# Kernel tuning notes

Measured on AMD Instinct MI355X. Metric: run time of the kernel, lower is better.

The kernel has to match this reference:

```python
import jax, jax.numpy as jnp
import numpy as np

N = 200000   # nodes
E = 6400000  # edges (avg degree 32)
T = 6        # member feature dim
M = 10       # fingerprint dim
L = 4        # R + 1 layers
GIN = 14     # group_level_input
GLO = 10     # group_level_output


def setup_inputs() -> dict:
    key = jax.random.key(0)
    ks = jax.random.split(key, 10)
    return {
        "x_member": jax.random.normal(ks[0], (N, T), dtype=jnp.float32),
        "x_group": jax.random.normal(ks[1], (1, GIN), dtype=jnp.float32),
        "src": jax.random.randint(ks[2], (E,), 0, N, dtype=jnp.int32),
        "dst": jax.random.randint(ks[3], (E,), 0, N, dtype=jnp.int32),
        "H": jax.random.normal(ks[4], (L, T, M), dtype=jnp.float32),
        "W": jax.random.normal(ks[5], (L,), dtype=jnp.float32),
        "gW": jax.random.normal(ks[6], (GLO, GIN), dtype=jnp.float32) * 0.1,
        "gb": jax.random.normal(ks[7], (GLO,), dtype=jnp.float32),
        "mW": jax.random.normal(ks[8], (3, M + GLO), dtype=jnp.float32) * 0.1,
        "mb": jax.random.normal(ks[9], (3,), dtype=jnp.float32),
    }


def reference(x_member, x_group, src, dst, H, W, gW, gb, mW, mb):
    n = x_member.shape[0]
    # message passing: neighbor feature sum per destination node  [N, T]
    neigh = jax.ops.segment_sum(x_member[src], dst, num_segments=n)
    v1 = x_member + neigh  # r[a] + sum of neighbor r's; r is layer-invariant
    # all R+1 layers at once: [L, N, M]
    v2 = jax.nn.sigmoid(jnp.einsum("nt,ltm->lnm", v1, H))
    fl = jax.nn.softmax(v2 * W[:, None, None], axis=-1)
    # f starts at zeros and accumulates softmax over every node and layer -> [1, M]
    f = jnp.sum(fl, axis=(0, 1))[None, :]
    # group-level perceptron
    g = jax.nn.sigmoid(x_group @ gW.T + gb)  # [1, GLO]
    merged = jnp.concatenate([f, g], axis=1)  # [1, M+GLO]
    return jax.nn.softmax(merged @ mW.T + mb, axis=-1)  # [1, 3]
```

## Files before the change

### kernel.cpp

```cpp
#include <hip/hip_runtime.h>
#include <hip/hip_fp16.h>
#include <math.h>

#define TDIM 6
#define MDIM 10
#define LDIM 4
#define GIND 14
#define GLOD 10

#define BINSHIFT 8
#define BINSZ 256
#define MAXBINS 1024

#define SC2_BLOCKS 512
#define SC2_THREADS 512
#define SC2_KQ 7
#define OVF_ENT 16384
#define META2 2048

#define SC_BLOCK 512
#define SC_EPT 32
#define SC_EPB (SC_BLOCK * SC_EPT)
#define AC_BLOCK 512
#define AC_CAP 8704
#define AC_EPT 17

__global__ void zero32_k(unsigned* __restrict__ p, int n) {
    int i = blockIdx.x * blockDim.x + threadIdx.x;
    if (i < n) p[i] = 0u;
}

__device__ __forceinline__ void add_row4(uint4 r, float& s0, float& s1, float& s2,
                                         float& s3, float& s4, float& s5) {
    float2 a0 = __half22float2(*(__half2*)&r.x);
    float2 a1 = __half22float2(*(__half2*)&r.y);
    float2 a2 = __half22float2(*(__half2*)&r.z);
    s0 += a0.x; s1 += a0.y; s2 += a1.x; s3 += a1.y; s4 += a2.x; s5 += a2.y;
}


__global__ __launch_bounds__(SC2_THREADS) void scat2_k(
        const float* __restrict__ xm, int N, uint4* __restrict__ xh,
        const int* __restrict__ src, const int* __restrict__ dst, int E, int NQ, int QPB,
        unsigned* __restrict__ gcount, unsigned* __restrict__ ebuf, int C, int nbins,
        uint2* __restrict__ ovf, unsigned* __restrict__ ocur) {
    __shared__ unsigned lcount[MAXBINS];
    __shared__ unsigned lbase[MAXBINS];
    int tid = threadIdx.x;
    for (int i = tid; i < MAXBINS; i += SC2_THREADS) lcount[i] = 0u;

    int gid = blockIdx.x * SC2_THREADS + tid;
    int gstride = gridDim.x * SC2_THREADS;
    for (int n = gid; n < N; n += gstride) {
        const float2* r = (const float2*)(xm + (size_t)n * TDIM);
        float2 a = r[0], b = r[1], c = r[2];
        __half2 h0 = __floats2half2_rn(a.x, a.y);
        __half2 h1 = __floats2half2_rn(b.x, b.y);
        __half2 h2 = __floats2half2_rn(c.x, c.y);
        uint4 o;
        o.x = *(unsigned*)&h0; o.y = *(unsigned*)&h1; o.z = *(unsigned*)&h2; o.w = 0u;
        xh[n] = o;
    }
    if (blockIdx.x == 0) {
        for (int e = NQ * 4 + tid; e < E; e += SC2_THREADS) {
            unsigned oc = atomicAdd(ocur, 1u);
            if (oc < OVF_ENT) ovf[oc] = make_uint2((unsigned)src[e], (unsigned)dst[e]);
        }
    }
    __syncthreads();

    int qb = blockIdx.x * QPB;
    int qend = qb + QPB; if (qend > NQ) qend = NQ;
    const int4* s4p = (const int4*)src;
    const int4* d4p = (const int4*)dst;

    unsigned pk[SC2_KQ * 4];
    unsigned wr[SC2_KQ * 4];

#pragma unroll
    for (int i = 0; i < SC2_KQ; i++) {
        int q = qb + tid + i * SC2_THREADS;
        if (q < qend) {
            int4 sv = s4p[q];
            int4 dv = d4p[q];
            {
                unsigned du = (unsigned)dv.x, b = du >> BINSHIFT;
                pk[i*4+0] = ((du & (BINSZ-1)) << 18) | (unsigned)sv.x;
                wr[i*4+0] = (b << 18) | atomicAdd(&lcount[b], 1u);
            }
            {
                unsigned du = (unsigned)dv.y, b = du >> BINSHIFT;
                pk[i*4+1] = ((du & (BINSZ-1)) << 18) | (unsigned)sv.y;
                wr[i*4+1] = (b << 18) | atomicAdd(&lcount[b], 1u);
            }
            {
                unsigned du = (unsigned)dv.z, b = du >> BINSHIFT;
                pk[i*4+2] = ((du & (BINSZ-1)) << 18) | (unsigned)sv.z;
                wr[i*4+2] = (b << 18) | atomicAdd(&lcount[b], 1u);
            }
            {
                unsigned du = (unsigned)dv.w, b = du >> BINSHIFT;
                pk[i*4+3] = ((du & (BINSZ-1)) << 18) | (unsigned)sv.w;
                wr[i*4+3] = (b << 18) | atomicAdd(&lcount[b], 1u);
            }
        } else {
            pk[i*4+0] = 0xFFFFFFFFu; pk[i*4+1] = 0xFFFFFFFFu;
            pk[i*4+2] = 0xFFFFFFFFu; pk[i*4+3] = 0xFFFFFFFFu;
        }
    }
    __syncthreads();

    for (int i = tid; i < nbins; i += SC2_THREADS) {
        unsigned c = lcount[i];
        if (c) lbase[i] = atomicAdd(&gcount[i], c);
    }
    __syncthreads();

#pragma unroll
    for (int k = 0; k < SC2_KQ * 4; k++) {
        unsigned p = pk[k];
        if (p != 0xFFFFFFFFu) {
            unsigned b = wr[k] >> 18;
            unsigned pos = lbase[b] + (wr[k] & 0x3FFFFu);
            if (pos < (unsigned)C) {
                ebuf[b * (unsigned)C + pos] = p;
            } else {
                unsigned oc = atomicAdd(ocur, 1u);
                if (oc < OVF_ENT) {
                    unsigned s = p & 0x3FFFFu;
                    unsigned d = (b << BINSHIFT) | (p >> 18);
                    ovf[oc] = make_uint2(s, d);
                }
            }
        }
    }
}

__global__ __launch_bounds__(AC_BLOCK) void accum2_k(
        const float* __restrict__ xm, const uint4* __restrict__ xh,
        const unsigned* __restrict__ ebuf, const unsigned* __restrict__ gcount, int C,
        const unsigned* __restrict__ ocur, const uint2* __restrict__ ovf,
        const float* __restrict__ H, const float* __restrict__ W,
        float* __restrict__ facc, int N) {
    __shared__ unsigned srt[AC_CAP];
    __shared__ unsigned cnt[BINSZ];
    __shared__ unsigned cstart[BINSZ];
    __shared__ unsigned wsum[8];
    __shared__ unsigned ovl[256];
    __shared__ unsigned ovn;
    __shared__ float sH[LDIM * TDIM * MDIM];
    __shared__ float sW[LDIM];
    __shared__ float sred[AC_BLOCK / 64][MDIM];
    __shared__ float part[2][BINSZ][TDIM];
    int tid = threadIdx.x;
    int bin = blockIdx.x;
    for (int i = tid; i < LDIM * TDIM * MDIM; i += AC_BLOCK) sH[i] = H[i];
    if (tid < LDIM) sW[tid] = W[tid];
    if (tid < BINSZ) cnt[tid] = 0u;
    if (tid == 0) ovn = 0u;
    __syncthreads();

    unsigned gc = gcount[bin];
    unsigned m = gc < (unsigned)C ? gc : (unsigned)C;
    unsigned e0 = (unsigned)bin * (unsigned)C;
    int nbase = bin << BINSHIFT;

    unsigned ed_[AC_EPT];
    unsigned rk_[AC_EPT];
#pragma unroll
    for (int k = 0; k < AC_EPT; k++) {
        unsigned i = (unsigned)tid + (unsigned)k * AC_BLOCK;
        if (i < m) {
            unsigned v = __builtin_nontemporal_load(ebuf + e0 + i);
            ed_[k] = v;
            rk_[k] = atomicAdd(&cnt[v >> 18], 1u);
        }
    }
    {
        unsigned novf = *ocur;
        if (novf > OVF_ENT) novf = OVF_ENT;
        for (unsigned i = tid; i < novf; i += AC_BLOCK) {
            uint2 e = ovf[i];
            if ((e.y >> BINSHIFT) == (unsigned)bin) {
                unsigned u = atomicAdd(&ovn, 1u);
                if (u < 256u) ovl[u] = ((e.y & (BINSZ-1)) << 18) | e.x;
            }
        }
    }
    __syncthreads();

    {
        unsigned v = (tid < BINSZ) ? cnt[tid] : 0u;
        int lane = tid & 63;
#pragma unroll
        for (int off = 1; off < 64; off <<= 1) {
            unsigned t = (unsigned)__shfl_up((int)v, off, 64);
            if (lane >= off) v += t;
        }
        if (tid < BINSZ && lane == 63) wsum[tid >> 6] = v;
        __syncthreads();
        if (tid < BINSZ) {
            unsigned add = 0;
            int w = tid >> 6;
#pragma unroll
            for (int ww = 0; ww < 3; ww++) if (ww < w) add += wsum[ww];
            cstart[tid] = v + add - cnt[tid];
        }
        __syncthreads();
    }

#pragma unroll
    for (int k = 0; k < AC_EPT; k++) {
        unsigned i = (unsigned)tid + (unsigned)k * AC_BLOCK;
        if (i < m) {
            unsigned v = ed_[k];
            srt[cstart[v >> 18] + rk_[k]] = v & 0x3FFFFu;
        }
    }
    __syncthreads();

    int node = tid & (BINSZ - 1);
    int role = tid >> 8;
    int n = nbase + node;
    float s0 = 0.f, s1 = 0.f, s2 = 0.f, s3 = 0.f, s4 = 0.f, s5 = 0.f;
    if (n < N) {
        unsigned c = cnt[node];
        unsigned b0 = cstart[node];
        unsigned h = c >> 1;
        unsigned j  = role ? h : 0u;
        unsigned je = role ? c : h;
        for (; j + 8 <= je; j += 8) {
            unsigned i0 = srt[b0 + j],     i1 = srt[b0 + j + 1];
            unsigned i2 = srt[b0 + j + 2], i3 = srt[b0 + j + 3];
            unsigned i4 = srt[b0 + j + 4], i5 = srt[b0 + j + 5];
            unsigned i6 = srt[b0 + j + 6], i7 = srt[b0 + j + 7];
            uint4 r0 = xh[i0], r1 = xh[i1], r2 = xh[i2], r3 = xh[i3];
            uint4 r4 = xh[i4], r5 = xh[i5], r6 = xh[i6], r7 = xh[i7];
            add_row4(r0, s0, s1, s2, s3, s4, s5);
            add_row4(r1, s0, s1, s2, s3, s4, s5);
            add_row4(r2, s0, s1, s2, s3, s4, s5);
            add_row4(r3, s0, s1, s2, s3, s4, s5);
            add_row4(r4, s0, s1, s2, s3, s4, s5);
            add_row4(r5, s0, s1, s2, s3, s4, s5);
            add_row4(r6, s0, s1, s2, s3, s4, s5);
            add_row4(r7, s0, s1, s2, s3, s4, s5);
        }
        for (; j + 2 <= je; j += 2) {
            unsigned ia = srt[b0 + j], ib = srt[b0 + j + 1];
            uint4 ra = xh[ia], rb = xh[ib];
            add_row4(ra, s0, s1, s2, s3, s4, s5);
            add_row4(rb, s0, s1, s2, s3, s4, s5);
        }
        if (j < je) {
            uint4 ra = xh[srt[b0 + j]];
            add_row4(ra, s0, s1, s2, s3, s4, s5);
        }
        if (role == 0) {
            unsigned no = ovn < 256u ? ovn : 256u;
            for (unsigned q = 0; q < no; q++) {
                unsigned o = ovl[q];
                if ((int)(o >> 18) == node) {
                    uint4 rr = xh[o & 0x3FFFFu];
                    add_row4(rr, s0, s1, s2, s3, s4, s5);
                }
            }
        }
    }
    part[role][node][0] = s0; part[role][node][1] = s1; part[role][node][2] = s2;
    part[role][node][3] = s3; part[role][node][4] = s4; part[role][node][5] = s5;
    __syncthreads();

    float fs[MDIM];
#pragma unroll
    for (int mm = 0; mm < MDIM; mm++) fs[mm] = 0.f;

    if (n < N) {
        float v[TDIM];
        const float2* xr = (const float2*)(xm + (size_t)n * TDIM);
        float2 x0 = xr[0], x1 = xr[1], x2 = xr[2];
        v[0] = x0.x + part[0][node][0] + part[1][node][0];
        v[1] = x0.y + part[0][node][1] + part[1][node][1];
        v[2] = x1.x + part[0][node][2] + part[1][node][2];
        v[3] = x1.y + part[0][node][3] + part[1][node][3];
        v[4] = x2.x + part[0][node][4] + part[1][node][4];
        v[5] = x2.y + part[0][node][5] + part[1][node][5];

        int lb = role << 1;
#pragma unroll
        for (int li = 0; li < 2; li++) {
            int l = lb + li;
            float z[MDIM];
#pragma unroll
            for (int mm = 0; mm < MDIM; mm++) {
                float a2 = 0.f;
#pragma unroll
                for (int t = 0; t < TDIM; t++) a2 += v[t] * sH[(l * TDIM + t) * MDIM + mm];
                z[mm] = a2;
            }
            float wl = sW[l];
            float mx = -1e30f;
#pragma unroll
            for (int mm = 0; mm < MDIM; mm++) {
                float sg = wl / (1.f + __expf(-z[mm]));
                z[mm] = sg;
                mx = fmaxf(mx, sg);
            }
            float se = 0.f;
#pragma unroll
            for (int mm = 0; mm < MDIM; mm++) {
                float e = __expf(z[mm] - mx);
                z[mm] = e;
                se += e;
            }
            float inv = 1.f / se;
#pragma unroll
            for (int mm = 0; mm < MDIM; mm++) fs[mm] += z[mm] * inv;
        }
    }

#pragma unroll
    for (int mm = 0; mm < MDIM; mm++) {
        float v = fs[mm];
#pragma unroll
        for (int off = 32; off > 0; off >>= 1) v += __shfl_down(v, off, 64);
        fs[mm] = v;
    }
    int wave = tid >> 6, lane = tid & 63;
    if (lane == 0) {
#pragma unroll
        for (int mm = 0; mm < MDIM; mm++) sred[wave][mm] = fs[mm];
    }
    __syncthreads();
    if (tid < MDIM) {
        float s = 0.f;
#pragma unroll
        for (int w = 0; w < AC_BLOCK / 64; w++) s += sred[w][tid];
        atomicAdd(facc + tid, s);
    }
}


__global__ __launch_bounds__(256) void prep_k(const float* __restrict__ xm, int N,
                                              uint4* __restrict__ xh,
                                              const int* __restrict__ dst, int E,
                                              unsigned* __restrict__ hist, int nbins) {
    __shared__ unsigned lh[MAXBINS];
    for (int i = threadIdx.x; i < MAXBINS; i += blockDim.x) lh[i] = 0u;
    __syncthreads();
    int gid = blockIdx.x * blockDim.x + threadIdx.x;
    int gstride = gridDim.x * blockDim.x;
    for (int n = gid; n < N; n += gstride) {
        const float2* r = (const float2*)(xm + (size_t)n * TDIM);
        float2 a = r[0], b = r[1], c = r[2];
        __half2 h0 = __floats2half2_rn(a.x, a.y);
        __half2 h1 = __floats2half2_rn(b.x, b.y);
        __half2 h2 = __floats2half2_rn(c.x, c.y);
        uint4 o;
        o.x = *(unsigned*)&h0; o.y = *(unsigned*)&h1; o.z = *(unsigned*)&h2; o.w = 0u;
        xh[n] = o;
    }
    int e4 = E >> 2;
    const int4* d4p = (const int4*)dst;
    for (int i = gid; i < e4; i += gstride) {
        int4 d = d4p[i];
        atomicAdd(&lh[((unsigned)d.x) >> BINSHIFT], 1u);
        atomicAdd(&lh[((unsigned)d.y) >> BINSHIFT], 1u);
        atomicAdd(&lh[((unsigned)d.z) >> BINSHIFT], 1u);
        atomicAdd(&lh[((unsigned)d.w) >> BINSHIFT], 1u);
    }
    for (int e = (e4 << 2) + gid; e < E; e += gstride)
        atomicAdd(&lh[((unsigned)dst[e]) >> BINSHIFT], 1u);
    __syncthreads();
    for (int i = threadIdx.x; i < nbins; i += blockDim.x)
        if (lh[i]) atomicAdd(&hist[i], lh[i]);
}

__global__ __launch_bounds__(MAXBINS) void scan_k(const unsigned* __restrict__ hist,
                                                  unsigned* __restrict__ offsets,
                                                  unsigned* __restrict__ gfill, int nbins) {
    __shared__ unsigned buf[2][MAXBINS];
    int t = threadIdx.x;
    buf[0][t] = (t < nbins) ? hist[t] : 0u;
    __syncthreads();
    int cur = 0;
    for (int off = 1; off < MAXBINS; off <<= 1) {
        unsigned v = buf[cur][t];
        if (t >= off) v += buf[cur][t - off];
        buf[cur ^ 1][t] = v;
        __syncthreads();
        cur ^= 1;
    }
    if (t < nbins) {
        unsigned ex = t ? buf[cur][t - 1] : 0u;
        offsets[t] = ex;
        gfill[t] = ex;
    }
    if (t == 0) offsets[nbins] = buf[cur][nbins - 1];
}

__global__ __launch_bounds__(SC_BLOCK) void scatter_k(const int* __restrict__ src,
                                                      const int* __restrict__ dst, int E,
                                                      unsigned* __restrict__ gfill,
                                                      unsigned* __restrict__ ebuf, int nbins) {
    __shared__ unsigned lcount[MAXBINS];
    __shared__ unsigned lbase[MAXBINS];
    for (int i = threadIdx.x; i < MAXBINS; i += SC_BLOCK) lcount[i] = 0u;
    __syncthreads();
    int base = blockIdx.x * SC_EPB + threadIdx.x * SC_EPT;
    int s[SC_EPT], d[SC_EPT];
    unsigned rk[SC_EPT];
#pragma unroll
    for (int q = 0; q < SC_EPT / 4; q++) {
        int e = base + q * 4;
        if (e + 3 < E) {
            int4 s4 = *(const int4*)(src + e);
            int4 d4 = *(const int4*)(dst + e);
            s[q*4+0] = s4.x; s[q*4+1] = s4.y; s[q*4+2] = s4.z; s[q*4+3] = s4.w;
            d[q*4+0] = d4.x; d[q*4+1] = d4.y; d[q*4+2] = d4.z; d[q*4+3] = d4.w;
        } else {
#pragma unroll
            for (int k = 0; k < 4; k++) {
                int ee = e + k;
                s[q*4+k] = (ee < E) ? src[ee] : -1;
                d[q*4+k] = (ee < E) ? dst[ee] : 0;
            }
        }
    }
#pragma unroll
    for (int k = 0; k < SC_EPT; k++)
        if (s[k] >= 0) rk[k] = atomicAdd(&lcount[((unsigned)d[k]) >> BINSHIFT], 1u);
    __syncthreads();
    for (int i = threadIdx.x; i < nbins; i += SC_BLOCK) {
        unsigned c = lcount[i];
        if (c) lbase[i] = atomicAdd(&gfill[i], c);
    }
    __syncthreads();
#pragma unroll
    for (int k = 0; k < SC_EPT; k++) {
        if (s[k] >= 0) {
            unsigned du = (unsigned)d[k];
            unsigned b = du >> BINSHIFT;
            unsigned pack = ((du & (BINSZ - 1)) << 18) | (unsigned)s[k];
            ebuf[lbase[b] + rk[k]] = pack;
        }
    }
}

__global__ __launch_bounds__(AC_BLOCK) void accum_node_k(
        const float* __restrict__ xm, const uint4* __restrict__ xh,
        const unsigned* __restrict__ ebuf, const unsigned* __restrict__ offsets,
        const float* __restrict__ H, const float* __restrict__ W,
        float* __restrict__ facc, int N) {
    __shared__ unsigned srt[AC_CAP];
    __shared__ unsigned cnt[BINSZ];
    __shared__ unsigned tmp[BINSZ];
    __shared__ unsigned cstart[BINSZ];
    __shared__ float sH[LDIM * TDIM * MDIM];
    __shared__ float sW[LDIM];
    __shared__ float sred[AC_BLOCK / 64][MDIM];
    int tid = threadIdx.x;
    int bin = blockIdx.x;
    for (int i = tid; i < LDIM * TDIM * MDIM; i += AC_BLOCK) sH[i] = H[i];
    if (tid < LDIM) sW[tid] = W[tid];
    if (tid < BINSZ) cnt[tid] = 0u;
    __syncthreads();

    unsigned e0 = offsets[bin], e1 = offsets[bin + 1];
    unsigned total = e1 - e0;
    unsigned m = total < AC_CAP ? total : AC_CAP;
    int nbase = bin << BINSHIFT;

    unsigned ed_[AC_EPT];
    unsigned rk_[AC_EPT];
#pragma unroll
    for (int k = 0; k < AC_EPT; k++) {
        unsigned idx = e0 + (unsigned)tid + (unsigned)k * AC_BLOCK;
        if (idx < e0 + m) {
            unsigned v = ebuf[idx];
            ed_[k] = v;
            rk_[k] = atomicAdd(&cnt[v >> 18], 1u);
        }
    }
    __syncthreads();

    if (tid < BINSZ) tmp[tid] = cnt[tid];
    __syncthreads();
    for (int off = 1; off < BINSZ; off <<= 1) {
        unsigned v = 0;
        if (tid < BINSZ) { v = tmp[tid]; if (tid >= off) v += tmp[tid - off]; }
        __syncthreads();
        if (tid < BINSZ) tmp[tid] = v;
        __syncthreads();
    }
    if (tid < BINSZ) cstart[tid] = tmp[tid] - cnt[tid];
    __syncthreads();

#pragma unroll
    for (int k = 0; k < AC_EPT; k++) {
        unsigned idx = e0 + (unsigned)tid + (unsigned)k * AC_BLOCK;
        if (idx < e0 + m) {
            unsigned v = ed_[k];
            srt[cstart[v >> 18] + rk_[k]] = v & 0x3FFFFu;
        }
    }
    __syncthreads();

    float fs[MDIM];
#pragma unroll
    for (int mm = 0; mm < MDIM; mm++) fs[mm] = 0.f;

    int n = nbase + tid;
    if (tid < BINSZ && n < N) {
        float s0 = 0.f, s1 = 0.f, s2 = 0.f, s3 = 0.f, s4 = 0.f, s5 = 0.f;
        unsigned c = cnt[tid];
        unsigned b0 = cstart[tid];
        unsigned j = 0;
        for (; j + 2 <= c; j += 2) {
            unsigned sa = srt[b0 + j], sb = srt[b0 + j + 1];
            uint4 ra = xh[sa];
            uint4 rb = xh[sb];
            add_row4(ra, s0, s1, s2, s3, s4, s5);
            add_row4(rb, s0, s1, s2, s3, s4, s5);
        }
        if (j < c) {
            uint4 ra = xh[srt[b0 + j]];
            add_row4(ra, s0, s1, s2, s3, s4, s5);
        }
        for (unsigned idx = e0 + m; idx < e1; idx++) {
            unsigned v = ebuf[idx];
            if ((int)(v >> 18) == tid) {
                uint4 ra = xh[v & 0x3FFFFu];
                add_row4(ra, s0, s1, s2, s3, s4, s5);
            }
        }

        float v[TDIM];
        const float2* xr = (const float2*)(xm + (size_t)n * TDIM);
        float2 x0 = xr[0], x1 = xr[1], x2 = xr[2];
        v[0] = x0.x + s0; v[1] = x0.y + s1;
        v[2] = x1.x + s2; v[3] = x1.y + s3;
        v[4] = x2.x + s4; v[5] = x2.y + s5;

#pragma unroll
        for (int l = 0; l < LDIM; l++) {
            float z[MDIM];
#pragma unroll
            for (int mm = 0; mm < MDIM; mm++) {
                float a2 = 0.f;
#pragma unroll
                for (int t = 0; t < TDIM; t++) a2 += v[t] * sH[(l * TDIM + t) * MDIM + mm];
                z[mm] = a2;
            }
            float wl = sW[l];
            float mx = -1e30f;
#pragma unroll
            for (int mm = 0; mm < MDIM; mm++) {
                float sg = wl / (1.f + __expf(-z[mm]));
                z[mm] = sg;
                mx = fmaxf(mx, sg);
            }
            float se = 0.f;
#pragma unroll
            for (int mm = 0; mm < MDIM; mm++) {
                float e = __expf(z[mm] - mx);
                z[mm] = e;
                se += e;
            }
            float inv = 1.f / se;
#pragma unroll
            for (int mm = 0; mm < MDIM; mm++) fs[mm] += z[mm] * inv;
        }
    }

#pragma unroll
    for (int mm = 0; mm < MDIM; mm++) {
        float v = fs[mm];
#pragma unroll
        for (int off = 32; off > 0; off >>= 1) v += __shfl_down(v, off, 64);
        fs[mm] = v;
    }
    int wave = tid >> 6, lane = tid & 63;
    if (lane == 0) {
#pragma unroll
        for (int mm = 0; mm < MDIM; mm++) sred[wave][mm] = fs[mm];
    }
    __syncthreads();
    if (tid < MDIM) {
        float s = 0.f;
#pragma unroll
        for (int w = 0; w < AC_BLOCK / 64; w++) s += sred[w][tid];
        atomicAdd(facc + tid, s);
    }
}

__global__ void finalize_k(const float* __restrict__ facc,
                           const float* __restrict__ xg,
                           const float* __restrict__ gW,
                           const float* __restrict__ gb,
                           const float* __restrict__ mW,
                           const float* __restrict__ mb,
                           float* __restrict__ out) {
    if (threadIdx.x == 0 && blockIdx.x == 0) {
        float merged[MDIM + GLOD];
#pragma unroll
        for (int m = 0; m < MDIM; m++) merged[m] = facc[m];
        for (int j = 0; j < GLOD; j++) {
            float a = gb[j];
            for (int i = 0; i < GIND; i++) a += xg[i] * gW[j * GIND + i];
            merged[MDIM + j] = 1.f / (1.f + __expf(-a));
        }
        float lg[3];
        float mx = -1e30f;
        for (int k = 0; k < 3; k++) {
            float a = mb[k];
            for (int j = 0; j < MDIM + GLOD; j++) a += merged[j] * mW[k * (MDIM + GLOD) + j];
            lg[k] = a;
            mx = fmaxf(mx, a);
        }
        float se = 0.f;
        for (int k = 0; k < 3; k++) { lg[k] = __expf(lg[k] - mx); se += lg[k]; }
        float inv = 1.f / se;
        for (int k = 0; k < 3; k++) out[k] = lg[k] * inv;
    }
}

__global__ void fb_zero_k(float* __restrict__ ws, int n) {
    int i = blockIdx.x * blockDim.x + threadIdx.x;
    if (i < n) ws[i] = 0.f;
}

__global__ void fb_edge_scatter_k(const float* __restrict__ xm,
                                  const int* __restrict__ src,
                                  const int* __restrict__ dst,
                                  float* __restrict__ neigh, int E) {
    int e = blockIdx.x * blockDim.x + threadIdx.x;
    if (e >= E) return;
    int s = src[e], d = dst[e];
    const float2* r = (const float2*)(xm + (size_t)s * TDIM);
    float2 a = r[0], b = r[1], c = r[2];
    float* o = neigh + (size_t)d * TDIM;
    atomicAdd(o + 0, a.x); atomicAdd(o + 1, a.y);
    atomicAdd(o + 2, b.x); atomicAdd(o + 3, b.y);
    atomicAdd(o + 4, c.x); atomicAdd(o + 5, c.y);
}

__global__ __launch_bounds__(256) void fb_node_k(
        const float* __restrict__ xm, const float* __restrict__ neigh,
        const float* __restrict__ H, const float* __restrict__ W,
        float* __restrict__ facc, int N) {
    __shared__ float sH[LDIM * TDIM * MDIM];
    __shared__ float sW[LDIM];
    __shared__ float sred[4][MDIM];
    int tid = threadIdx.x;
    for (int i = tid; i < LDIM * TDIM * MDIM; i += blockDim.x) sH[i] = H[i];
    if (tid < LDIM) sW[tid] = W[tid];
    __syncthreads();
    float fs[MDIM];
#pragma unroll
    for (int m = 0; m < MDIM; m++) fs[m] = 0.f;
    for (int n = blockIdx.x * blockDim.x + tid; n < N; n += gridDim.x * blockDim.x) {
        float v[TDIM];
        const float2* xr = (const float2*)(xm + (size_t)n * TDIM);
        const float2* nr = (const float2*)(neigh + (size_t)n * TDIM);
#pragma unroll
        for (int t2 = 0; t2 < 3; t2++) {
            float2 a = xr[t2], b = nr[t2];
            v[2 * t2 + 0] = a.x + b.x;
            v[2 * t2 + 1] = a.y + b.y;
        }
#pragma unroll
        for (int l = 0; l < LDIM; l++) {
            float z[MDIM];
#pragma unroll
            for (int m = 0; m < MDIM; m++) {
                float a2 = 0.f;
#pragma unroll
                for (int t = 0; t < TDIM; t++) a2 += v[t] * sH[(l * TDIM + t) * MDIM + m];
                z[m] = a2;
            }
            float wl = sW[l], mx = -1e30f;
#pragma unroll
            for (int m = 0; m < MDIM; m++) { float sg = wl / (1.f + __expf(-z[m])); z[m] = sg; mx = fmaxf(mx, sg); }
            float se = 0.f;
#pragma unroll
            for (int m = 0; m < MDIM; m++) { float e = __expf(z[m] - mx); z[m] = e; se += e; }
            float inv = 1.f / se;
#pragma unroll
            for (int m = 0; m < MDIM; m++) fs[m] += z[m] * inv;
        }
    }
#pragma unroll
    for (int m = 0; m < MDIM; m++) {
        float v = fs[m];
#pragma unroll
        for (int off = 32; off > 0; off >>= 1) v += __shfl_down(v, off, 64);
        fs[m] = v;
    }
    int wave = tid >> 6, lane = tid & 63;
    if (lane == 0) {
#pragma unroll
        for (int m = 0; m < MDIM; m++) sred[wave][m] = fs[m];
    }
    __syncthreads();
    if (tid < MDIM) {
        float s = sred[0][tid] + sred[1][tid] + sred[2][tid] + sred[3][tid];
        atomicAdd(facc + tid, s);
    }
}

extern "C" void kernel_launch(void* const* d_in, const int* in_sizes, int n_in,
                              void* d_out, int out_size, void* d_ws, size_t ws_size,
                              hipStream_t stream) {
    const float* xm  = (const float*)d_in[0];
    const float* xg  = (const float*)d_in[1];
    const int*   src = (const int*)d_in[2];
    const int*   dst = (const int*)d_in[3];
    const float* H   = (const float*)d_in[4];
    const float* W   = (const float*)d_in[5];
    const float* gW  = (const float*)d_in[6];
    const float* gb  = (const float*)d_in[7];
    const float* mW  = (const float*)d_in[8];
    const float* mb  = (const float*)d_in[9];
    float* out = (float*)d_out;

    int N = in_sizes[0] / TDIM;
    int E = in_sizes[2];
    int nbins = (N + BINSZ - 1) >> BINSHIFT;
    size_t ws_words = ws_size / 4;
    size_t xh_words = (size_t)N * 4;

    long fixed = (long)(xh_words + META2 + (size_t)OVF_ENT * 2);
    long avail = (long)ws_words - fixed;
    long C = avail > 0 ? (avail / nbins) & ~3L : 0;
    if (C > AC_CAP) C = AC_CAP;
    double mu = (double)E / nbins;
    long Cmin = (long)(mu + 4.0 * sqrt(mu) + 32.0);
    int NQ = E >> 2;
    int QPB = (NQ + SC2_BLOCKS - 1) / SC2_BLOCKS;
    bool ok1 = (C >= Cmin) && nbins <= MAXBINS && N <= (1 << 18) &&
               QPB <= SC2_KQ * SC2_THREADS;

    size_t meta_words2 = MAXBINS + (MAXBINS + 1) + MAXBINS + 16;
    size_t need2 = (xh_words + (size_t)E + meta_words2) * 4;
    bool ok2 = ws_size >= need2 && nbins <= MAXBINS && N <= (1 << 18);

    if (ok1) {
        uint4*    xh     = (uint4*)d_ws;
        unsigned* ebuf   = (unsigned*)d_ws + xh_words;
        unsigned* gcount = ebuf + (size_t)nbins * C;
        unsigned* ocur   = gcount + MAXBINS;
        float*    facc   = (float*)(ocur + 16);
        uint2*    ovf    = (uint2*)(gcount + META2);

        zero32_k<<<(META2 + 255) / 256, 256, 0, stream>>>(gcount, META2);
        scat2_k<<<SC2_BLOCKS, SC2_THREADS, 0, stream>>>(xm, N, xh, src, dst, E, NQ, QPB,
                                                        gcount, ebuf, (int)C, nbins, ovf, ocur);
        accum2_k<<<nbins, AC_BLOCK, 0, stream>>>(xm, xh, ebuf, gcount, (int)C, ocur, ovf,
                                                 H, W, facc, N);
        finalize_k<<<1, 64, 0, stream>>>(facc, xg, gW, gb, mW, mb, out);
    } else if (ok2) {
        uint4*    xh      = (uint4*)d_ws;
        unsigned* ebuf    = (unsigned*)d_ws + xh_words;
        unsigned* hist    = ebuf + (size_t)E;
        unsigned* offsets = hist + MAXBINS;
        unsigned* gfill   = offsets + MAXBINS + 1;
        float*    facc    = (float*)(gfill + MAXBINS);

        zero32_k<<<(int)((meta_words2 + 255) / 256), 256, 0, stream>>>(hist, (int)meta_words2);
        prep_k<<<1024, 256, 0, stream>>>(xm, N, xh, dst, E, hist, nbins);
        scan_k<<<1, MAXBINS, 0, stream>>>(hist, offsets, gfill, nbins);
        scatter_k<<<(E + SC_EPB - 1) / SC_EPB, SC_BLOCK, 0, stream>>>(src, dst, E, gfill, ebuf, nbins);
        accum_node_k<<<nbins, AC_BLOCK, 0, stream>>>(xm, xh, ebuf, offsets, H, W, facc, N);
        finalize_k<<<1, 64, 0, stream>>>(facc, xg, gW, gb, mW, mb, out);
    } else {
        float* neigh = (float*)d_ws;
        float* facc  = neigh + (size_t)N * TDIM;
        int zn = N * TDIM + 16;
        fb_zero_k<<<(zn + 255) / 256, 256, 0, stream>>>(neigh, zn);
        fb_edge_scatter_k<<<(E + 255) / 256, 256, 0, stream>>>(xm, src, dst, neigh, E);
        fb_node_k<<<256, 256, 0, stream>>>(xm, neigh, H, W, facc, N);
        finalize_k<<<1, 64, 0, stream>>>(facc, xg, gW, gb, mW, mb, out);
    }
}
```

Measured before the change: 135.2 us.

## Halve bin size and split each node's edges across four threads

Bins shrink from 256 to 128 nodes, doubling the number of bins and accum blocks, with shared sort capacity and per-thread edge slots scaled down to match. Each node is now handled by four threads: each gathers a quarter of the node's neighbor list and then computes one of the four layers. This is meant to raise parallelism and cut the per-thread gather latency chain and shared memory per block. The scan kernel is rewritten to handle two bins per thread so it can cover 2048 bins. It risks a higher overflow rate because per-bin capacity headroom changes, plus more blocks and more scatter-stage metadata.

Result: slower. 148.7 us (+9.9%).

```diff
diff --git a/kernel.cpp b/kernel.cpp
--- a/kernel.cpp
+++ b/kernel.cpp
@@ -8,22 +8,22 @@
 #define GIND 14
 #define GLOD 10
 
-#define BINSHIFT 8
-#define BINSZ 256
-#define MAXBINS 1024
+#define BINSHIFT 7
+#define BINSZ 128
+#define MAXBINS 2048
 
 #define SC2_BLOCKS 512
 #define SC2_THREADS 512
 #define SC2_KQ 7
 #define OVF_ENT 16384
-#define META2 2048
+#define META2 4096
 
 #define SC_BLOCK 512
 #define SC_EPT 32
 #define SC_EPB (SC_BLOCK * SC_EPT)
 #define AC_BLOCK 512
-#define AC_CAP 8704
-#define AC_EPT 17
+#define AC_CAP 4480
+#define AC_EPT 9
 
 __global__ void zero32_k(unsigned* __restrict__ p, int n) {
     int i = blockIdx.x * blockDim.x + threadIdx.x;
@@ -145,13 +145,13 @@
     __shared__ unsigned srt[AC_CAP];
     __shared__ unsigned cnt[BINSZ];
     __shared__ unsigned cstart[BINSZ];
-    __shared__ unsigned wsum[8];
+    __shared__ unsigned wsum[BINSZ / 64];
     __shared__ unsigned ovl[256];
     __shared__ unsigned ovn;
     __shared__ float sH[LDIM * TDIM * MDIM];
     __shared__ float sW[LDIM];
     __shared__ float sred[AC_BLOCK / 64][MDIM];
-    __shared__ float part[2][BINSZ][TDIM];
+    __shared__ float part[4][BINSZ][TDIM];
     int tid = threadIdx.x;
     int bin = blockIdx.x;
     for (int i = tid; i < LDIM * TDIM * MDIM; i += AC_BLOCK) sH[i] = H[i];
@@ -203,7 +203,7 @@
             unsigned add = 0;
             int w = tid >> 6;
 #pragma unroll
-            for (int ww = 0; ww < 3; ww++) if (ww < w) add += wsum[ww];
+            for (int ww = 0; ww < BINSZ / 64 - 1; ww++) if (ww < w) add += wsum[ww];
             cstart[tid] = v + add - cnt[tid];
         }
         __syncthreads();
@@ -220,38 +220,24 @@
     __syncthreads();
 
     int node = tid & (BINSZ - 1);
-    int role = tid >> 8;
+    int role = tid >> 7;
     int n = nbase + node;
     float s0 = 0.f, s1 = 0.f, s2 = 0.f, s3 = 0.f, s4 = 0.f, s5 = 0.f;
     if (n < N) {
         unsigned c = cnt[node];
         unsigned b0 = cstart[node];
-        unsigned h = c >> 1;
-        unsigned j  = role ? h : 0u;
-        unsigned je = role ? c : h;
-        for (; j + 8 <= je; j += 8) {
+        unsigned j  = (c * (unsigned)role) >> 2;
+        unsigned je = (c * (unsigned)(role + 1)) >> 2;
+        for (; j + 4 <= je; j += 4) {
             unsigned i0 = srt[b0 + j],     i1 = srt[b0 + j + 1];
             unsigned i2 = srt[b0 + j + 2], i3 = srt[b0 + j + 3];
-            unsigned i4 = srt[b0 + j + 4], i5 = srt[b0 + j + 5];
-            unsigned i6 = srt[b0 + j + 6], i7 = srt[b0 + j + 7];
             uint4 r0 = xh[i0], r1 = xh[i1], r2 = xh[i2], r3 = xh[i3];
-            uint4 r4 = xh[i4], r5 = xh[i5], r6 = xh[i6], r7 = xh[i7];
             add_row4(r0, s0, s1, s2, s3, s4, s5);
             add_row4(r1, s0, s1, s2, s3, s4, s5);
             add_row4(r2, s0, s1, s2, s3, s4, s5);
             add_row4(r3, s0, s1, s2, s3, s4, s5);
-            add_row4(r4, s0, s1, s2, s3, s4, s5);
-            add_row4(r5, s0, s1, s2, s3, s4, s5);
-            add_row4(r6, s0, s1, s2, s3, s4, s5);
-            add_row4(r7, s0, s1, s2, s3, s4, s5);
-        }
-        for (; j + 2 <= je; j += 2) {
-            unsigned ia = srt[b0 + j], ib = srt[b0 + j + 1];
-            uint4 ra = xh[ia], rb = xh[ib];
-            add_row4(ra, s0, s1, s2, s3, s4, s5);
-            add_row4(rb, s0, s1, s2, s3, s4, s5);
-        }
-        if (j < je) {
+        }
+        for (; j < je; ++j) {
             uint4 ra = xh[srt[b0 + j]];
             add_row4(ra, s0, s1, s2, s3, s4, s5);
         }
@@ -278,44 +264,40 @@
         float v[TDIM];
         const float2* xr = (const float2*)(xm + (size_t)n * TDIM);
         float2 x0 = xr[0], x1 = xr[1], x2 = xr[2];
-        v[0] = x0.x + part[0][node][0] + part[1][node][0];
-        v[1] = x0.y + part[0][node][1] + part[1][node][1];
-        v[2] = x1.x + part[0][node][2] + part[1][node][2];
-        v[3] = x1.y + part[0][node][3] + part[1][node][3];
-        v[4] = x2.x + part[0][node][4] + part[1][node][4];
-        v[5] = x2.y + part[0][node][5] + part[1][node][5];
-
-        int lb = role << 1;
-#pragma unroll
-        for (int li = 0; li < 2; li++) {
-            int l = lb + li;
-            float z[MDIM];
-#pragma unroll
-            for (int mm = 0; mm < MDIM; mm++) {
-                float a2 = 0.f;
-#pragma unroll
-                for (int t = 0; t < TDIM; t++) a2 += v[t] * sH[(l * TDIM + t) * MDIM + mm];
-                z[mm] = a2;
-            }
-            float wl = sW[l];
-            float mx = -1e30f;
-#pragma unroll
-            for (int mm = 0; mm < MDIM; mm++) {
-                float sg = wl / (1.f + __expf(-z[mm]));
-                z[mm] = sg;
-                mx = fmaxf(mx, sg);
-            }
-            float se = 0.f;
-#pragma unroll
-            for (int mm = 0; mm < MDIM; mm++) {
-                float e = __expf(z[mm] - mx);
-                z[mm] = e;
-                se += e;
-            }
-            float inv = 1.f / se;
-#pragma unroll
-            for (int mm = 0; mm < MDIM; mm++) fs[mm] += z[mm] * inv;
-        }
+        v[0] = x0.x + part[0][node][0] + part[1][node][0] + part[2][node][0] + part[3][node][0];
+        v[1] = x0.y + part[0][node][1] + part[1][node][1] + part[2][node][1] + part[3][node][1];
+        v[2] = x1.x + part[0][node][2] + part[1][node][2] + part[2][node][2] + part[3][node][2];
+        v[3] = x1.y + part[0][node][3] + part[1][node][3] + part[2][node][3] + part[3][node][3];
+        v[4] = x2.x + part[0][node][4] + part[1][node][4] + part[2][node][4] + part[3][node][4];
+        v[5] = x2.y + part[0][node][5] + part[1][node][5] + part[2][node][5] + part[3][node][5];
+
+        int l = role;
+        float z[MDIM];
+#pragma unroll
+        for (int mm = 0; mm < MDIM; mm++) {
+            float a2 = 0.f;
+#pragma unroll
+            for (int t = 0; t < TDIM; t++) a2 += v[t] * sH[(l * TDIM + t) * MDIM + mm];
+            z[mm] = a2;
+        }
+        float wl = sW[l];
+        float mx = -1e30f;
+#pragma unroll
+        for (int mm = 0; mm < MDIM; mm++) {
+            float sg = wl / (1.f + __expf(-z[mm]));
+            z[mm] = sg;
+            mx = fmaxf(mx, sg);
+        }
+        float se = 0.f;
+#pragma unroll
+        for (int mm = 0; mm < MDIM; mm++) {
+            float e = __expf(z[mm] - mx);
+            z[mm] = e;
+            se += e;
+        }
+        float inv = 1.f / se;
+#pragma unroll
+        for (int mm = 0; mm < MDIM; mm++) fs[mm] += z[mm] * inv;
     }
 
 #pragma unroll
@@ -375,27 +357,28 @@
         if (lh[i]) atomicAdd(&hist[i], lh[i]);
 }
 
-__global__ __launch_bounds__(MAXBINS) void scan_k(const unsigned* __restrict__ hist,
-                                                  unsigned* __restrict__ offsets,
-                                                  unsigned* __restrict__ gfill, int nbins) {
-    __shared__ unsigned buf[2][MAXBINS];
+__global__ __launch_bounds__(1024) void scan_k(const unsigned* __restrict__ hist,
+                                               unsigned* __restrict__ offsets,
+                                               unsigned* __restrict__ gfill, int nbins) {
+    __shared__ unsigned buf[2][1024];
     int t = threadIdx.x;
-    buf[0][t] = (t < nbins) ? hist[t] : 0u;
+    unsigned a = (2 * t < nbins) ? hist[2 * t] : 0u;
+    unsigned b = (2 * t + 1 < nbins) ? hist[2 * t + 1] : 0u;
+    buf[0][t] = a + b;
     __syncthreads();
     int cur = 0;
-    for (int off = 1; off < MAXBINS; off <<= 1) {
+    for (int off = 1; off < 1024; off <<= 1) {
         unsigned v = buf[cur][t];
         if (t >= off) v += buf[cur][t - off];
         buf[cur ^ 1][t] = v;
         __syncthreads();
         cur ^= 1;
     }
-    if (t < nbins) {
-        unsigned ex = t ? buf[cur][t - 1] : 0u;
-        offsets[t] = ex;
-        gfill[t] = ex;
-    }
-    if (t == 0) offsets[nbins] = buf[cur][nbins - 1];
+    unsigned incl = buf[cur][t];
+    unsigned exclp = incl - (a + b);
+    if (2 * t < nbins)     { offsets[2 * t]     = exclp;     gfill[2 * t]     = exclp; }
+    if (2 * t + 1 < nbins) { offsets[2 * t + 1] = exclp + a; gfill[2 * t + 1] = exclp + a; }
+    if (t == 1023) offsets[nbins] = buf[cur][1023];
 }
 
 __global__ __launch_bounds__(SC_BLOCK) void scatter_k(const int* __restrict__ src,
@@ -768,7 +751,7 @@
 
         zero32_k<<<(int)((meta_words2 + 255) / 256), 256, 0, stream>>>(hist, (int)meta_words2);
         prep_k<<<1024, 256, 0, stream>>>(xm, N, xh, dst, E, hist, nbins);
-        scan_k<<<1, MAXBINS, 0, stream>>>(hist, offsets, gfill, nbins);
+        scan_k<<<1, 1024, 0, stream>>>(hist, offsets, gfill, nbins);
         scatter_k<<<(E + SC_EPB - 1) / SC_EPB, SC_BLOCK, 0, stream>>>(src, dst, E, gfill, ebuf, nbins);
         accum_node_k<<<nbins, AC_BLOCK, 0, stream>>>(xm, xh, ebuf, offsets, H, W, facc, N);
         finalize_k<<<1, 64, 0, stream>>>(facc, xg, gW, gb, mW, mb, out);
```
